# Performance work log

Hardware: AMD Instinct MI355X
Metric: run time of the kernel (lower is better)

The kernel has to match this reference:

```python
import jax, jax.numpy as jnp
import numpy as np
from jax import lax

VOCAB = 100   # chars_count
E = 32        # CHARACTER_EMBEDDING_SIZE
H = 64        # CHAR_LSTM_HIDDEN_SIZE
N_WORDS = 65536
MAX_LEN = 16


def setup_inputs() -> dict:
    key = jax.random.key(0)
    k_ch, k_len, k_emb, k_wih, k_whh, k_bih, k_bhh = jax.random.split(key, 7)
    chars = jax.random.randint(k_ch, (N_WORDS, MAX_LEN), 0, VOCAB, dtype=jnp.int32)
    lengths = jax.random.randint(k_len, (N_WORDS,), 1, MAX_LEN + 1, dtype=jnp.int32)
    s = 1.0 / np.sqrt(H)  # torch LSTM default init scale
    emb = jax.random.normal(k_emb, (VOCAB, E), dtype=jnp.float32)
    W_ih = jax.random.uniform(k_wih, (4 * H, E), minval=-s, maxval=s, dtype=jnp.float32)
    W_hh = jax.random.uniform(k_whh, (4 * H, H), minval=-s, maxval=s, dtype=jnp.float32)
    b_ih = jax.random.uniform(k_bih, (4 * H,), minval=-s, maxval=s, dtype=jnp.float32)
    b_hh = jax.random.uniform(k_bhh, (4 * H,), minval=-s, maxval=s, dtype=jnp.float32)
    return {"emb": emb, "W_ih": W_ih, "W_hh": W_hh, "b_ih": b_ih, "b_hh": b_hh,
            "chars": chars, "lengths": lengths}


def _char_lstm(emb, W_ih, W_hh, b_ih, b_hh, chars, lengths):
    N, L = chars.shape
    h0 = jnp.zeros((N, H), dtype=emb.dtype)
    c0 = jnp.zeros((N, H), dtype=emb.dtype)

    def step(carry, inp):
        h, c = carry
        ch_t, t = inp  # ch_t: [N] char ids at timestep t
        x = emb[ch_t]  # [N, E]
        gates = x @ W_ih.T + b_ih + h @ W_hh.T + b_hh  # [N, 4H]
        i_g, f_g, g_g, o_g = jnp.split(gates, 4, axis=-1)  # torch order i,f,g,o
        i_g = jax.nn.sigmoid(i_g)
        f_g = jax.nn.sigmoid(f_g)
        g_g = jnp.tanh(g_g)
        o_g = jax.nn.sigmoid(o_g)
        c_new = f_g * c + i_g * g_g
        h_new = o_g * jnp.tanh(c_new)
        active = (t < lengths)[:, None]  # freeze state past word end -> out[-1]
        h = jnp.where(active, h_new, h)
        c = jnp.where(active, c_new, c)
        return (h, c), None

    (h_final, _), _ = lax.scan(step, (h0, c0), (chars.T, jnp.arange(L)))
    return h_final  # [N, H] = last valid hidden per word


def reference(emb, W_ih, W_hh, b_ih, b_hh, chars, lengths):
    return _char_lstm(emb, W_ih, W_hh, b_ih, b_hh, chars, lengths)
```

## Files before the change

### kernel.cpp

```cpp
#include <hip/hip_runtime.h>
#include <hip/hip_bf16.h>


#define VOCAB 100
#define E     32
#define NW    65536
#define MAXL  16
#define NGRP  4096

typedef __bf16 bf16x8 __attribute__((ext_vector_type(8)));
typedef float  f32x4  __attribute__((ext_vector_type(4)));
typedef unsigned short ushort_t;
typedef unsigned int uint_t;

#define LOG2E    1.4426950408889634f
#define TWOLOG2E 2.8853900817779268f

__device__ __forceinline__ ushort_t f2bf(float x) {
    union { __hip_bfloat16 b; ushort_t u; } cv;
    cv.b = __float2bfloat16(x);
    return cv.u;
}
__device__ __forceinline__ float exp2_hw(float x) { return __builtin_amdgcn_exp2f(x); }
__device__ __forceinline__ float rcp_hw(float x)  { return __builtin_amdgcn_rcpf(x); }

__global__ void prep_all(const float* __restrict__ emb, const float* __restrict__ Wih,
                         const float* __restrict__ Whh, const float* __restrict__ bih,
                         const float* __restrict__ bhh, const int* __restrict__ lengths,
                         float* __restrict__ xtab, ushort_t* __restrict__ Wb,
                         int* __restrict__ bh) {
    int bid = blockIdx.x;
    if (bid < VOCAB) {
        int ch = bid, g = threadIdx.x, q = g >> 6;
        float scl = (q == 2) ? TWOLOG2E : -LOG2E;
        float acc = bih[g] + bhh[g];
        const float* er = emb + ch * E;
        const float* wr = Wih + g * E;
        #pragma unroll
        for (int e = 0; e < E; ++e) acc = fmaf(er[e], wr[e], acc);
        xtab[ch * 256 + g] = acc * scl;
    } else if (bid < VOCAB + 64) {
        int i = (bid - VOCAB) * 256 + threadIdx.x;
        int q = i >> 12;
        float scl = (q == 2) ? TWOLOG2E : -LOG2E;
        Wb[i] = f2bf(Whh[i] * scl);
    } else {
        int blk = bid - (VOCAB + 64);
        __shared__ int h[16];
        if (threadIdx.x < 16) h[threadIdx.x] = 0;
        __syncthreads();
        atomicAdd(&h[lengths[blk * 256 + threadIdx.x] - 1], 1);
        __syncthreads();
        if (threadIdx.x < 16) bh[blk * 16 + threadIdx.x] = h[threadIdx.x];
    }
}

__global__ void k_sort(const int* __restrict__ lengths, const int* __restrict__ bh,
                       int* __restrict__ perm) {
    __shared__ int lbh[4096];
    __shared__ int pre[16], tot[16], gb[16], mybase[16], hh[16];
    const int t = threadIdx.x, B = blockIdx.x;
    for (int i = t; i < 4096; i += 256) lbh[i] = bh[i];
    if (t < 16) hh[t] = 0;
    __syncthreads();
    if (t < 16) {
        int s = 0;
        for (int B2 = 0; B2 < B; ++B2) s += lbh[B2 * 16 + t];
        int tt = s;
        for (int B2 = B; B2 < 256; ++B2) tt += lbh[B2 * 16 + t];
        pre[t] = s; tot[t] = tt;
    }
    __syncthreads();
    if (t == 0) { int a = 0; for (int i = 0; i < 16; ++i) { gb[i] = a; a += tot[i]; } }
    __syncthreads();
    if (t < 16) mybase[t] = gb[t] + pre[t];
    __syncthreads();
    int w = B * 256 + t;
    int b = lengths[w] - 1;
    int r = atomicAdd(&hh[b], 1);
    perm[mybase[b] + r] = w;
}

__global__ __launch_bounds__(256, 2) void lstm_main(
    const ushort_t* __restrict__ Wb, const float* __restrict__ xtab,
    const int* __restrict__ chars, const int* __restrict__ lengths,
    const int* __restrict__ perm, float* __restrict__ out)
{
    __shared__ __align__(16) char Hlds_all[4][2048];
    char* Hbase = Hlds_all[threadIdx.x >> 6];

    const int lane = threadIdx.x & 63;
    const int w  = lane & 15;
    const int lq = lane >> 4;
    const int wave = (blockIdx.x << 2) + (threadIdx.x >> 6);

    bf16x8 a[16][2];
    #pragma unroll
    for (int m = 0; m < 16; ++m)
        #pragma unroll
        for (int kh = 0; kh < 2; ++kh)
            a[m][kh] = *reinterpret_cast<const bf16x8*>(Wb + ((m * 16 + w) * 64 + kh * 32 + lq * 8));

    const int sw = (w & 7) << 4;
    const int base_w = w * 128;
    int wr_off[4], rd_off[2];
    #pragma unroll
    for (int b = 0; b < 4; ++b) wr_off[b] = base_w + ((b * 32 + lq * 8) ^ sw);
    #pragma unroll
    for (int kh = 0; kh < 2; ++kh) rd_off[kh] = base_w + ((kh * 64 + lq * 16) ^ sw);

    #pragma unroll 1
    for (int gi = 0; gi < 2; ++gi) {
        const int grp = gi ? (NGRP - 1 - wave) : wave;
        const int wid = perm[grp * 16 + w];
        const int len = lengths[wid];
        int ml = len;
        ml = max(ml, __shfl_xor(ml, 1));
        ml = max(ml, __shfl_xor(ml, 2));
        ml = max(ml, __shfl_xor(ml, 4));
        ml = max(ml, __shfl_xor(ml, 8));
        const int maxl = __builtin_amdgcn_readfirstlane(ml);
        const int* chp = chars + wid * MAXL;

        float hreg[4][4], creg[4][4];
        #pragma unroll
        for (int b = 0; b < 4; ++b)
            #pragma unroll
            for (int r = 0; r < 4; ++r) { hreg[b][r] = 0.f; creg[b][r] = 0.f; }

        int ch = chp[0];
        const float* xrow = xtab + ch * 256;
        f32x4 xtb[2][4];
        #pragma unroll
        for (int q = 0; q < 4; ++q)
            xtb[0][q] = *reinterpret_cast<const f32x4*>(xrow + (q * 4 + 0) * 16 + lq * 4);

        #pragma unroll 1
        for (int t = 0; t < maxl; ++t) {
            const int tn = (t + 1 < maxl) ? t + 1 : t;
            const int ch_nxt = chp[tn];
            const float* xrow_n = xtab + ch_nxt * 256;

            bf16x8 B0, B1;
            if (t > 0) {
                asm volatile("s_waitcnt lgkmcnt(0)" ::: "memory");
                B0 = *reinterpret_cast<const bf16x8*>(Hbase + rd_off[0]);
                B1 = *reinterpret_cast<const bf16x8*>(Hbase + rd_off[1]);
            }
            const bool act = (t < len);

            #pragma unroll
            for (int b = 0; b < 4; ++b) {
                if (b < 3) {
                    #pragma unroll
                    for (int q = 0; q < 4; ++q)
                        xtb[(b + 1) & 1][q] = *reinterpret_cast<const f32x4*>(xrow + (q * 4 + b + 1) * 16 + lq * 4);
                } else {
                    #pragma unroll
                    for (int q = 0; q < 4; ++q)
                        xtb[0][q] = *reinterpret_cast<const f32x4*>(xrow_n + q * 64 + lq * 4);
                }
                f32x4 d[4];
                #pragma unroll
                for (int q = 0; q < 4; ++q) d[q] = xtb[b & 1][q];
                if (t > 0) {
                    #pragma unroll
                    for (int q = 0; q < 4; ++q) {
                        d[q] = __builtin_amdgcn_mfma_f32_16x16x32_bf16(a[q * 4 + b][0], B0, d[q], 0, 0, 0);
                        d[q] = __builtin_amdgcn_mfma_f32_16x16x32_bf16(a[q * 4 + b][1], B1, d[q], 0, 0, 0);
                    }
                }
                #pragma unroll
                for (int r = 0; r < 4; ++r) {
                    float ui = exp2_hw(d[0][r]);
                    float uf = exp2_hw(d[1][r]);
                    float ug = exp2_hw(d[2][r]);
                    float uo = exp2_hw(d[3][r]);
                    float ti = 1.f + ui, tg = 1.f + ug;
                    float igg = (ug - 1.f) * rcp_hw(ti * tg);
                    float fg  = rcp_hw(1.f + uf);
                    float cn  = fmaf(fg, creg[b][r], igg);
                    float uc  = exp2_hw(cn * TWOLOG2E);
                    float to  = 1.f + uo, tc = 1.f + uc;
                    float hn  = (uc - 1.f) * rcp_hw(to * tc);
                    creg[b][r] = act ? cn : creg[b][r];
                    hreg[b][r] = act ? hn : hreg[b][r];
                }
                uint_t lo = (uint_t)f2bf(hreg[b][0]) | ((uint_t)f2bf(hreg[b][1]) << 16);
                uint_t hi = (uint_t)f2bf(hreg[b][2]) | ((uint_t)f2bf(hreg[b][3]) << 16);
                *reinterpret_cast<uint2*>(Hbase + wr_off[b]) = make_uint2(lo, hi);
            }
            ch = ch_nxt;
            xrow = xrow_n;
        }

        #pragma unroll
        for (int b = 0; b < 4; ++b) {
            f32x4 o;
            #pragma unroll
            for (int r = 0; r < 4; ++r) o[r] = hreg[b][r];
            *reinterpret_cast<f32x4*>(out + wid * 64 + b * 16 + lq * 4) = o;
        }
    }
}

extern "C" void kernel_launch(void* const* d_in, const int* in_sizes, int n_in,
                              void* d_out, int out_size, void* d_ws, size_t ws_size,
                              hipStream_t stream) {
    const float* emb = (const float*)d_in[0];
    const float* Wih = (const float*)d_in[1];
    const float* Whh = (const float*)d_in[2];
    const float* bih = (const float*)d_in[3];
    const float* bhh = (const float*)d_in[4];
    const int* chars = (const int*)d_in[5];
    const int* lens  = (const int*)d_in[6];
    float* out = (float*)d_out;

    float*    xtab = (float*)d_ws;
    ushort_t* Wb   = (ushort_t*)(xtab + 25600);
    int*      bh   = (int*)(Wb + 16384);
    int*      perm = bh + 4096;

    prep_all<<<VOCAB + 64 + 256, 256, 0, stream>>>(emb, Wih, Whh, bih, bhh, lens, xtab, Wb, bh);
    k_sort<<<256, 256, 0, stream>>>(lens, bh, perm);

    lstm_main<<<512, 256, 0, stream>>>(Wb, xtab, chars, lens, perm, out);
}
```

Before: 155.5 us.

## Process gate blocks in pairs and prefetch the next step's input row

Restructures the LSTM timestep loop to handle two 16-column gate blocks per inner iteration, so eight independent MFMA chains and batched exp/rcp evaluations can interleave. The x-projection table row for step t+1 is loaded in full during step t, with the char id fetched two steps ahead. The LDS read of the new hidden state moves to the end of each step instead of the start. The aim is more instruction-level parallelism and hidden global-load latency on the serial recurrence. It costs more registers, which at two blocks per SM may cause spills or lower occupancy.

```diff
diff --git a/kernel.cpp b/kernel.cpp
--- a/kernel.cpp
+++ b/kernel.cpp
@@ -128,70 +128,115 @@
             #pragma unroll
             for (int r = 0; r < 4; ++r) { hreg[b][r] = 0.f; creg[b][r] = 0.f; }
 
-        int ch = chp[0];
-        const float* xrow = xtab + ch * 256;
-        f32x4 xtb[2][4];
-        #pragma unroll
-        for (int q = 0; q < 4; ++q)
-            xtb[0][q] = *reinterpret_cast<const f32x4*>(xrow + (q * 4 + 0) * 16 + lq * 4);
+        int chA = chp[0];
+        int chB = chp[maxl > 1 ? 1 : 0];
+        f32x4 xtb[2][4][2];
+        {
+            const float* xr = xtab + chA * 256;
+            #pragma unroll
+            for (int bp = 0; bp < 2; ++bp)
+                #pragma unroll
+                for (int q = 0; q < 4; ++q)
+                    #pragma unroll
+                    for (int bi = 0; bi < 2; ++bi)
+                        xtb[bp][q][bi] = *reinterpret_cast<const f32x4*>(xr + (q * 4 + bp * 2 + bi) * 16 + lq * 4);
+        }
+
+        bf16x8 Bc0, Bc1;
 
         #pragma unroll 1
         for (int t = 0; t < maxl; ++t) {
-            const int tn = (t + 1 < maxl) ? t + 1 : t;
-            const int ch_nxt = chp[tn];
-            const float* xrow_n = xtab + ch_nxt * 256;
-
-            bf16x8 B0, B1;
-            if (t > 0) {
-                asm volatile("s_waitcnt lgkmcnt(0)" ::: "memory");
-                B0 = *reinterpret_cast<const bf16x8*>(Hbase + rd_off[0]);
-                B1 = *reinterpret_cast<const bf16x8*>(Hbase + rd_off[1]);
+            const int tnn = (t + 2 < maxl) ? t + 2 : maxl - 1;
+            const int chC = chp[tnn];
+            const float* xrow_n = xtab + chB * 256;
+            const bool act = (t < len);
+
+            #pragma unroll
+            for (int bp = 0; bp < 2; ++bp) {
+                f32x4 dd[4][2];
+                #pragma unroll
+                for (int q = 0; q < 4; ++q)
+                    #pragma unroll
+                    for (int bi = 0; bi < 2; ++bi)
+                        dd[q][bi] = xtb[bp][q][bi];
+                if (t > 0) {
+                    #pragma unroll
+                    for (int q = 0; q < 4; ++q)
+                        #pragma unroll
+                        for (int bi = 0; bi < 2; ++bi) {
+                            dd[q][bi] = __builtin_amdgcn_mfma_f32_16x16x32_bf16(a[q * 4 + bp * 2 + bi][0], Bc0, dd[q][bi], 0, 0, 0);
+                            dd[q][bi] = __builtin_amdgcn_mfma_f32_16x16x32_bf16(a[q * 4 + bp * 2 + bi][1], Bc1, dd[q][bi], 0, 0, 0);
+                        }
+                }
+                #pragma unroll
+                for (int q = 0; q < 4; ++q)
+                    #pragma unroll
+                    for (int bi = 0; bi < 2; ++bi)
+                        xtb[bp][q][bi] = *reinterpret_cast<const f32x4*>(xrow_n + (q * 4 + bp * 2 + bi) * 16 + lq * 4);
+
+                float ui[2][4], uf[2][4], ug[2][4], uo[2][4];
+                #pragma unroll
+                for (int bi = 0; bi < 2; ++bi)
+                    #pragma unroll
+                    for (int r = 0; r < 4; ++r) ui[bi][r] = exp2_hw(dd[0][bi][r]);
+                #pragma unroll
+                for (int bi = 0; bi < 2; ++bi)
+                    #pragma unroll
+                    for (int r = 0; r < 4; ++r) uf[bi][r] = exp2_hw(dd[1][bi][r]);
+                #pragma unroll
+                for (int bi = 0; bi < 2; ++bi)
+                    #pragma unroll
+                    for (int r = 0; r < 4; ++r) ug[bi][r] = exp2_hw(dd[2][bi][r]);
+                #pragma unroll
+                for (int bi = 0; bi < 2; ++bi)
+                    #pragma unroll
+                    for (int r = 0; r < 4; ++r) uo[bi][r] = exp2_hw(dd[3][bi][r]);
+
+                float igg[2][4], fg[2][4];
+                #pragma unroll
+                for (int bi = 0; bi < 2; ++bi)
+                    #pragma unroll
+                    for (int r = 0; r < 4; ++r)
+                        igg[bi][r] = (ug[bi][r] - 1.f) * rcp_hw((1.f + ui[bi][r]) * (1.f + ug[bi][r]));
+                #pragma unroll
+                for (int bi = 0; bi < 2; ++bi)
+                    #pragma unroll
+                    for (int r = 0; r < 4; ++r) fg[bi][r] = rcp_hw(1.f + uf[bi][r]);
+
+                float cnl[2][4];
+                #pragma unroll
+                for (int bi = 0; bi < 2; ++bi)
+                    #pragma unroll
+                    for (int r = 0; r < 4; ++r)
+                        cnl[bi][r] = fmaf(fg[bi][r], creg[bp * 2 + bi][r], igg[bi][r]);
+
+                float uc[2][4];
+                #pragma unroll
+                for (int bi = 0; bi < 2; ++bi)
+                    #pragma unroll
+                    for (int r = 0; r < 4; ++r) uc[bi][r] = exp2_hw(cnl[bi][r] * TWOLOG2E);
+
+                #pragma unroll
+                for (int bi = 0; bi < 2; ++bi) {
+                    const int b = bp * 2 + bi;
+                    #pragma unroll
+                    for (int r = 0; r < 4; ++r) {
+                        float hn = (uc[bi][r] - 1.f) * rcp_hw((1.f + uo[bi][r]) * (1.f + uc[bi][r]));
+                        creg[b][r] = act ? cnl[bi][r] : creg[b][r];
+                        hreg[b][r] = act ? hn : hreg[b][r];
+                    }
+                    uint_t lo = (uint_t)f2bf(hreg[b][0]) | ((uint_t)f2bf(hreg[b][1]) << 16);
+                    uint_t hi = (uint_t)f2bf(hreg[b][2]) | ((uint_t)f2bf(hreg[b][3]) << 16);
+                    *reinterpret_cast<uint2*>(Hbase + wr_off[b]) = make_uint2(lo, hi);
+                }
             }
-            const bool act = (t < len);
-
-            #pragma unroll
-            for (int b = 0; b < 4; ++b) {
-                if (b < 3) {
-                    #pragma unroll
-                    for (int q = 0; q < 4; ++q)
-                        xtb[(b + 1) & 1][q] = *reinterpret_cast<const f32x4*>(xrow + (q * 4 + b + 1) * 16 + lq * 4);
-                } else {
-                    #pragma unroll
-                    for (int q = 0; q < 4; ++q)
-                        xtb[0][q] = *reinterpret_cast<const f32x4*>(xrow_n + q * 64 + lq * 4);
-                }
-                f32x4 d[4];
-                #pragma unroll
-                for (int q = 0; q < 4; ++q) d[q] = xtb[b & 1][q];
-                if (t > 0) {
-                    #pragma unroll
-                    for (int q = 0; q < 4; ++q) {
-                        d[q] = __builtin_amdgcn_mfma_f32_16x16x32_bf16(a[q * 4 + b][0], B0, d[q], 0, 0, 0);
-                        d[q] = __builtin_amdgcn_mfma_f32_16x16x32_bf16(a[q * 4 + b][1], B1, d[q], 0, 0, 0);
-                    }
-                }
-                #pragma unroll
-                for (int r = 0; r < 4; ++r) {
-                    float ui = exp2_hw(d[0][r]);
-                    float uf = exp2_hw(d[1][r]);
-                    float ug = exp2_hw(d[2][r]);
-                    float uo = exp2_hw(d[3][r]);
-                    float ti = 1.f + ui, tg = 1.f + ug;
-                    float igg = (ug - 1.f) * rcp_hw(ti * tg);
-                    float fg  = rcp_hw(1.f + uf);
-                    float cn  = fmaf(fg, creg[b][r], igg);
-                    float uc  = exp2_hw(cn * TWOLOG2E);
-                    float to  = 1.f + uo, tc = 1.f + uc;
-                    float hn  = (uc - 1.f) * rcp_hw(to * tc);
-                    creg[b][r] = act ? cn : creg[b][r];
-                    hreg[b][r] = act ? hn : hreg[b][r];
-                }
-                uint_t lo = (uint_t)f2bf(hreg[b][0]) | ((uint_t)f2bf(hreg[b][1]) << 16);
-                uint_t hi = (uint_t)f2bf(hreg[b][2]) | ((uint_t)f2bf(hreg[b][3]) << 16);
-                *reinterpret_cast<uint2*>(Hbase + wr_off[b]) = make_uint2(lo, hi);
-            }
-            ch = ch_nxt;
-            xrow = xrow_n;
+
+            asm volatile("s_waitcnt lgkmcnt(0)" ::: "memory");
+            Bc0 = *reinterpret_cast<const bf16x8*>(Hbase + rd_off[0]);
+            Bc1 = *reinterpret_cast<const bf16x8*>(Hbase + rd_off[1]);
+
+            chA = chB;
+            chB = chC;
         }
 
         #pragma unroll
```

Measured after the change: 202.7 us. 1.3x slower.
